# Kernel optimization log

Measured on AMD Instinct MI355X. Metric: run time of the kernel, lower is better.

Reference implementation:

```python
import jax, jax.numpy as jnp
import numpy as np

WINDOW_SIZE = 11
SIGMA = 1.5
C1 = 0.01 ** 2
C2 = 0.03 ** 2


def _gaussian_window(window_size, sigma, channel):
    xs = np.arange(window_size)
    g = np.exp(-((xs - window_size // 2) ** 2) / (2.0 * sigma ** 2))
    g = (g / g.sum()).astype(np.float32)
    w2d = np.outer(g, g)  # [k,k]
    # depthwise kernel layout OIHW with O=channel, I=1
    return jnp.asarray(np.broadcast_to(w2d, (channel, 1, window_size, window_size)).copy())


def _blur(x, window, channel):
    # depthwise conv, SAME-style padding = k//2 (k odd -> exact SAME)
    pad = WINDOW_SIZE // 2
    return jax.lax.conv_general_dilated(
        x, window,
        window_strides=(1, 1),
        padding=[(pad, pad), (pad, pad)],
        dimension_numbers=('NCHW', 'OIHW', 'NCHW'),
        feature_group_count=channel,
    )


def setup_inputs() -> dict:
    key = jax.random.key(0)
    k1, k2 = jax.random.split(key)
    shape = (32, 3, 512, 512)
    img1 = jax.random.uniform(k1, shape, dtype=jnp.float32)
    img2 = jax.random.uniform(k2, shape, dtype=jnp.float32)
    return {"img1": img1, "img2": img2}


def reference(img1, img2):
    channel = img1.shape[1]
    window = _gaussian_window(WINDOW_SIZE, SIGMA, channel).astype(img1.dtype)

    mu1 = _blur(img1, window, channel)
    mu2 = _blur(img2, window, channel)
    mu1_sq = mu1 * mu1
    mu2_sq = mu2 * mu2
    mu1_mu2 = mu1 * mu2

    sigma1_sq = _blur(img1 * img1, window, channel) - mu1_sq
    sigma2_sq = _blur(img2 * img2, window, channel) - mu2_sq
    sigma12 = _blur(img1 * img2, window, channel) - mu1_mu2

    ssim_map = ((2 * mu1_mu2 + C1) * (2 * sigma12 + C2)) / (
        (mu1_sq + mu2_sq + C1) * (sigma1_sq + sigma2_sq + C2))
    return 1.0 - jnp.mean(ssim_map)
```

## Files before the change

### kernel.cpp

```cpp
#include <hip/hip_runtime.h>


#define HH 512
#define WW 512
#define TILE 32
#define IN_ROWS 42
#define S_STRIDE 50
#define H_STRIDE 34
#define NPLANES 96
#define NPIX 25165824.0f
#define NACC 256
#define NTASK 672

#define H01_OFF 0
#define H23_OFF 11424
#define H4_OFF  22848
#define UNION_BYTES 28560

typedef float v2f __attribute__((ext_vector_type(2)));
typedef float v4f __attribute__((ext_vector_type(4)));

__global__ __launch_bounds__(256, 5) void ssim_fused_kernel(
    const float* __restrict__ img1, const float* __restrict__ img2,
    float* __restrict__ acc) {
  __shared__ __align__(16) char ub[UNION_BYTES];
  __shared__ float wsum[4];

  v2f (*s12)[S_STRIDE] = (v2f (*)[S_STRIDE])ub;
  v2f (*h01)[H_STRIDE] = (v2f (*)[H_STRIDE])(ub + H01_OFF);
  v2f (*h23)[H_STRIDE] = (v2f (*)[H_STRIDE])(ub + H23_OFF);
  float (*h4)[H_STRIDE] = (float (*)[H_STRIDE])(ub + H4_OFF);

  const int tid = threadIdx.x;
  const int tx = blockIdx.x * TILE;
  const int ty = blockIdx.y * TILE;
  const size_t base = (size_t)blockIdx.z * (HH * WW);

  const float g[11] = {
      1.0283800e-03f, 7.5987600e-03f, 3.6000770e-02f, 1.0936072e-01f,
      2.1300560e-01f, 2.6601170e-01f, 2.1300560e-01f, 1.0936072e-01f,
      3.6000770e-02f, 7.5987600e-03f, 1.0283800e-03f};

#pragma unroll
  for (int it = 0; it < 2; ++it) {
    int idx = it * 256 + tid;
    if (idx < IN_ROWS * 12) {
      int r = idx / 12;
      int p = idx - r * 12;
      int gy = ty - 5 + r;
      int gx = tx - 8 + 4 * p;
      v4f A = {0.f, 0.f, 0.f, 0.f}, B = {0.f, 0.f, 0.f, 0.f};
      if ((unsigned)gy < (unsigned)HH && (unsigned)gx < (unsigned)WW) {
        size_t off = base + (size_t)gy * WW + gx;
        A = *(const v4f*)(img1 + off);
        B = *(const v4f*)(img2 + off);
      }
      *(v4f*)&s12[r][4 * p]     = (v4f){A.x, B.x, A.y, B.y};
      *(v4f*)&s12[r][4 * p + 2] = (v4f){A.z, B.z, A.w, B.w};
    }
  }
  __syncthreads();

  v2f hold01[3][2], hold23[3][2], hold4[3];
#pragma unroll
  for (int t = 0; t < 3; ++t) {
    int idx = t * 256 + tid;
    if (idx < NTASK) {
      int r = idx >> 4;
      int c = (idx & 15) * 2;
      const v4f* qp = (const v4f*)&s12[r][c + 2];
      v4f q0 = qp[0], q1 = qp[1], q2 = qp[2], q3 = qp[3];
      v4f q4 = qp[4], q5 = qp[5], q6 = qp[6];
      v2f P[14];
      P[0]  = (v2f){q0.x, q0.y};  P[1]  = (v2f){q0.z, q0.w};
      P[2]  = (v2f){q1.x, q1.y};  P[3]  = (v2f){q1.z, q1.w};
      P[4]  = (v2f){q2.x, q2.y};  P[5]  = (v2f){q2.z, q2.w};
      P[6]  = (v2f){q3.x, q3.y};  P[7]  = (v2f){q3.z, q3.w};
      P[8]  = (v2f){q4.x, q4.y};  P[9]  = (v2f){q4.z, q4.w};
      P[10] = (v2f){q5.x, q5.y};  P[11] = (v2f){q5.z, q5.w};
      P[12] = (v2f){q6.x, q6.y};  P[13] = (v2f){q6.z, q6.w};

      v2f a01_0 = (v2f){0.f, 0.f}, a23_0 = (v2f){0.f, 0.f};
      v2f a01_1 = (v2f){0.f, 0.f}, a23_1 = (v2f){0.f, 0.f};
      float a4_0 = 0.f, a4_1 = 0.f;
#pragma unroll
      for (int dx = 0; dx < 11; ++dx) {
        float w = g[dx];
        v2f v0 = P[1 + dx];
        v2f v1 = P[2 + dx];
        a01_0 += w * v0;
        a01_1 += w * v1;
        a23_0 += w * (v0 * v0);
        a23_1 += w * (v1 * v1);
        a4_0 = __builtin_fmaf(w, v0.x * v0.y, a4_0);
        a4_1 = __builtin_fmaf(w, v1.x * v1.y, a4_1);
      }
      hold01[t][0] = a01_0;  hold01[t][1] = a01_1;
      hold23[t][0] = a23_0;  hold23[t][1] = a23_1;
      hold4[t] = (v2f){a4_0, a4_1};
    }
  }
  __syncthreads();

#pragma unroll
  for (int t = 0; t < 3; ++t) {
    int idx = t * 256 + tid;
    if (idx < NTASK) {
      int r = idx >> 4;
      int c = (idx & 15) * 2;
      *(v4f*)&h01[r][c] = (v4f){hold01[t][0].x, hold01[t][0].y,
                                hold01[t][1].x, hold01[t][1].y};
      *(v4f*)&h23[r][c] = (v4f){hold23[t][0].x, hold23[t][0].y,
                                hold23[t][1].x, hold23[t][1].y};
      *(v2f*)&h4[r][c] = hold4[t];
    }
  }
  __syncthreads();

  const float C1 = 1e-4f;
  const float C2 = 9e-4f;
  const int c = tid & 31;
  const int r0 = (tid >> 5) * 4;

  v2f m[4], vv[4];
  float b12[4];
#pragma unroll
  for (int o = 0; o < 4; ++o) {
    m[o] = (v2f){0.f, 0.f};
    vv[o] = (v2f){0.f, 0.f};
    b12[o] = 0.f;
  }

#pragma unroll
  for (int dy = 0; dy < 14; ++dy) {
    v2f a = h01[r0 + dy][c];
    v2f b = h23[r0 + dy][c];
    float d = h4[r0 + dy][c];
#pragma unroll
    for (int o = 0; o < 4; ++o) {
      const int k = dy - o;
      if (k >= 0 && k < 11) {
        float w = g[k];
        m[o] += w * a;
        vv[o] += w * b;
        b12[o] = __builtin_fmaf(w, d, b12[o]);
      }
    }
  }

  float lsum = 0.f;
#pragma unroll
  for (int o = 0; o < 4; ++o) {
    float mu1 = m[o].x, mu2 = m[o].y;
    float mu1sq = mu1 * mu1;
    float mu2sq = mu2 * mu2;
    float mu12 = mu1 * mu2;
    float sig11 = vv[o].x - mu1sq;
    float sig22 = vv[o].y - mu2sq;
    float sig12 = b12[o] - mu12;
    float num = (2.f * mu12 + C1) * (2.f * sig12 + C2);
    float den = (mu1sq + mu2sq + C1) * (sig11 + sig22 + C2);
    lsum += num * __builtin_amdgcn_rcpf(den);
  }

#pragma unroll
  for (int off = 32; off > 0; off >>= 1)
    lsum += __shfl_down(lsum, off, 64);
  const int lane = tid & 63;
  const int wid = tid >> 6;
  if (lane == 0) wsum[wid] = lsum;
  __syncthreads();
  if (tid == 0) {
    float b = wsum[0] + wsum[1] + wsum[2] + wsum[3];
    int slot = (blockIdx.x + blockIdx.y * 16 + blockIdx.z) & (NACC - 1);
    atomicAdd(acc + slot, b);
  }
}

__global__ void ssim_finalize_kernel(const float* __restrict__ acc,
                                     float* __restrict__ out) {
  __shared__ float wsum[4];
  const int tid = threadIdx.x;
  float s = acc[tid];
#pragma unroll
  for (int off = 32; off > 0; off >>= 1)
    s += __shfl_down(s, off, 64);
  if ((tid & 63) == 0) wsum[tid >> 6] = s;
  __syncthreads();
  if (tid == 0)
    out[0] = 1.0f - (wsum[0] + wsum[1] + wsum[2] + wsum[3]) * (1.0f / NPIX);
}

extern "C" void kernel_launch(void* const* d_in, const int* in_sizes, int n_in,
                              void* d_out, int out_size, void* d_ws, size_t ws_size,
                              hipStream_t stream) {
  const float* img1 = (const float*)d_in[0];
  const float* img2 = (const float*)d_in[1];
  float* out = (float*)d_out;
  float* acc = (float*)d_ws;

  (void)hipMemsetAsync(acc, 0, NACC * sizeof(float), stream);

  dim3 grid(WW / TILE, HH / TILE, NPLANES);
  ssim_fused_kernel<<<grid, 256, 0, stream>>>(img1, img2, acc);
  ssim_finalize_kernel<<<1, NACC, 0, stream>>>(acc, out);
}
```

Baseline: 276.9 us.

## Interleave horizontal blur outputs into v4f layout and dedupe squared products

The horizontal-pass intermediates for means and second moments are merged into one interleaved float4 array with stride 32, so the vertical pass reads them with one 16-byte LDS load per row instead of two 8-byte loads. The horizontal loop now computes squares and cross products once per input sample and shares them between the two output columns, removing redundant multiplies. The smaller LDS footprint allows the launch bound to rise to 6 blocks per CU, which may add register pressure. Dropping the padded stride can introduce LDS bank conflicts.

```diff
diff --git a/kernel.cpp b/kernel.cpp
--- a/kernel.cpp
+++ b/kernel.cpp
@@ -6,29 +6,27 @@
 #define TILE 32
 #define IN_ROWS 42
 #define S_STRIDE 50
-#define H_STRIDE 34
+#define H_STRIDE 32
 #define NPLANES 96
 #define NPIX 25165824.0f
 #define NACC 256
 #define NTASK 672
 
-#define H01_OFF 0
-#define H23_OFF 11424
-#define H4_OFF  22848
-#define UNION_BYTES 28560
+#define H0123_OFF 0
+#define H4_OFF  21504
+#define UNION_BYTES 26880
 
 typedef float v2f __attribute__((ext_vector_type(2)));
 typedef float v4f __attribute__((ext_vector_type(4)));
 
-__global__ __launch_bounds__(256, 5) void ssim_fused_kernel(
+__global__ __launch_bounds__(256, 6) void ssim_fused_kernel(
     const float* __restrict__ img1, const float* __restrict__ img2,
     float* __restrict__ acc) {
   __shared__ __align__(16) char ub[UNION_BYTES];
   __shared__ float wsum[4];
 
   v2f (*s12)[S_STRIDE] = (v2f (*)[S_STRIDE])ub;
-  v2f (*h01)[H_STRIDE] = (v2f (*)[H_STRIDE])(ub + H01_OFF);
-  v2f (*h23)[H_STRIDE] = (v2f (*)[H_STRIDE])(ub + H23_OFF);
+  v4f (*h0123)[H_STRIDE] = (v4f (*)[H_STRIDE])(ub + H0123_OFF);
   float (*h4)[H_STRIDE] = (float (*)[H_STRIDE])(ub + H4_OFF);
 
   const int tid = threadIdx.x;
@@ -84,16 +82,22 @@
       v2f a01_1 = (v2f){0.f, 0.f}, a23_1 = (v2f){0.f, 0.f};
       float a4_0 = 0.f, a4_1 = 0.f;
 #pragma unroll
-      for (int dx = 0; dx < 11; ++dx) {
-        float w = g[dx];
-        v2f v0 = P[1 + dx];
-        v2f v1 = P[2 + dx];
-        a01_0 += w * v0;
-        a01_1 += w * v1;
-        a23_0 += w * (v0 * v0);
-        a23_1 += w * (v1 * v1);
-        a4_0 = __builtin_fmaf(w, v0.x * v0.y, a4_0);
-        a4_1 = __builtin_fmaf(w, v1.x * v1.y, a4_1);
+      for (int k = 1; k <= 12; ++k) {
+        v2f p = P[k];
+        v2f sq = p * p;
+        float cr = p.x * p.y;
+        if (k <= 11) {
+          float w = g[k - 1];
+          a01_0 += w * p;
+          a23_0 += w * sq;
+          a4_0 = __builtin_fmaf(w, cr, a4_0);
+        }
+        if (k >= 2) {
+          float w = g[k - 2];
+          a01_1 += w * p;
+          a23_1 += w * sq;
+          a4_1 = __builtin_fmaf(w, cr, a4_1);
+        }
       }
       hold01[t][0] = a01_0;  hold01[t][1] = a01_1;
       hold23[t][0] = a23_0;  hold23[t][1] = a23_1;
@@ -108,10 +112,10 @@
     if (idx < NTASK) {
       int r = idx >> 4;
       int c = (idx & 15) * 2;
-      *(v4f*)&h01[r][c] = (v4f){hold01[t][0].x, hold01[t][0].y,
-                                hold01[t][1].x, hold01[t][1].y};
-      *(v4f*)&h23[r][c] = (v4f){hold23[t][0].x, hold23[t][0].y,
-                                hold23[t][1].x, hold23[t][1].y};
+      *(v4f*)&h0123[r][c]     = (v4f){hold01[t][0].x, hold01[t][0].y,
+                                      hold23[t][0].x, hold23[t][0].y};
+      *(v4f*)&h0123[r][c + 1] = (v4f){hold01[t][1].x, hold01[t][1].y,
+                                      hold23[t][1].x, hold23[t][1].y};
       *(v2f*)&h4[r][c] = hold4[t];
     }
   }
@@ -133,8 +137,9 @@
 
 #pragma unroll
   for (int dy = 0; dy < 14; ++dy) {
-    v2f a = h01[r0 + dy][c];
-    v2f b = h23[r0 + dy][c];
+    v4f q = h0123[r0 + dy][c];
+    v2f a = (v2f){q.x, q.y};
+    v2f b = (v2f){q.z, q.w};
     float d = h4[r0 + dy][c];
 #pragma unroll
     for (int o = 0; o < 4; ++o) {
```

Result: no change. 279.7 us (+1.0%).
